# Kernel tuning notes

Measured on AMD Instinct MI355X. Metric: run time of the kernel, lower is better.

The kernel has to match this reference:

```python
import jax, jax.numpy as jnp
import numpy as np

NEG = -1e30       # log-space 'zero'
KD_FACTOR = 0.5   # self.kd_factor
KD_TEMP = 1.0     # self.kd_temp is never set in the original __init__; use 1.0
BLANK = 0         # torch CTCLoss default blank id


def ctc_loss(logits, targets, ilens, olens):
    """CTC negative log-likelihood, sum-reduced / B (matches builtin path:
    log_softmax + nn.CTCLoss(reduction='sum', zero_infinity=True) / batch).
    logits: [B,T,C]; targets: [B,L] label ids (no blanks); ilens, olens: [B]."""
    B, T, C = logits.shape
    L = targets.shape[1]
    S = 2 * L + 1
    lp = jax.nn.log_softmax(logits, axis=-1)                     # [B,T,C]
    # extended label sequence: blank, y1, blank, y2, ..., blank  -> [B,S]
    ext = jnp.zeros((B, S), dtype=targets.dtype).at[:, 1::2].set(targets)
    prev2 = jnp.pad(ext, ((0, 0), (2, 0)))[:, :S]
    allow2 = (ext != BLANK) & (ext != prev2) & (jnp.arange(S)[None, :] >= 2)
    # per-frame emission log-probs of extended labels: [T,B,S]
    emit = jnp.take_along_axis(lp, jnp.broadcast_to(ext[:, None, :], (B, T, S)), axis=2)
    emit = jnp.transpose(emit, (1, 0, 2))
    alpha0 = (jnp.full((B, S), NEG, dtype=lp.dtype)
              .at[:, 0].set(emit[0, :, 0])
              .at[:, 1].set(emit[0, :, 1]))

    def step(alpha, xs):
        e_t, t = xs
        s1 = jnp.pad(alpha, ((0, 0), (1, 0)), constant_values=NEG)[:, :S]
        s2 = jnp.where(allow2, jnp.pad(alpha, ((0, 0), (2, 0)), constant_values=NEG)[:, :S], NEG)
        m = jnp.maximum(jnp.maximum(alpha, s1), s2)
        new = m + jnp.log(jnp.exp(alpha - m) + jnp.exp(s1 - m) + jnp.exp(s2 - m)) + e_t
        # freeze alpha past each sample's input length -> alpha at t = ilen-1
        new = jnp.where((t < ilens)[:, None], new, alpha)
        return new, None

    alpha, _ = jax.lax.scan(step, alpha0, (emit[1:], jnp.arange(1, T)))
    end = 2 * olens                                              # last blank index
    bidx = jnp.arange(B)
    ll = jnp.logaddexp(alpha[bidx, end], alpha[bidx, end - 1])
    loss = -ll
    loss = jnp.where(loss > 1e20, 0.0, loss)                     # zero_infinity
    return loss.sum() / B


def kd_loss(logits, soft_logits, hlens):
    """Vectorized form of the per-sample ragged KD loop:
    sum_b -(softmax(soft[b,:h]/T) * log_softmax(logits[b,:h]/T)).sum() / B."""
    B, T, _ = logits.shape
    p = jax.nn.softmax(soft_logits / KD_TEMP, axis=-1)
    logq = jax.nn.log_softmax(logits / KD_TEMP, axis=-1)
    cxe = -(p * logq).sum(-1)                                    # [B,T]
    mask = jnp.arange(T)[None, :] < hlens[:, None]
    return jnp.where(mask, cxe, 0.0).sum() / B


def setup_inputs() -> dict:
    key = jax.random.key(0)
    k1, k2, k3, k4, k5, k6 = jax.random.split(key, 6)
    B, T, E, V, L = 16, 512, 512, 5000, 64
    hs_pad = jax.random.normal(k1, (B, T, E), jnp.float32)
    soft_logits = jax.random.normal(k2, (B, T, V), jnp.float32)
    W = jax.random.normal(k3, (E, V), jnp.float32) * 0.02
    b = jnp.zeros((V,), jnp.float32)
    hlens = jax.random.randint(k4, (B,), 300, T + 1)             # T >= 2L+1 guaranteed
    targets = jax.random.randint(k5, (B, L), 1, V)               # no blank labels
    olens = jax.random.randint(k6, (B,), 32, L + 1)
    return {"hs_pad": hs_pad, "soft_logits": soft_logits, "W": W, "b": b,
            "hlens": hlens, "targets": targets, "olens": olens}


def reference(hs_pad, soft_logits, W, b, hlens, targets, olens):
    # ctc_lo(F.dropout(hs_pad, p=0.0)) -> plain linear projection
    logits = hs_pad @ W + b                                      # [B,T,V]
    loss_ctc = ctc_loss(logits, targets, hlens, olens)
    loss_kd = kd_loss(logits, soft_logits, hlens)
    return KD_FACTOR * loss_kd + (1.0 - KD_FACTOR) * loss_ctc
```

## Files before the change

### kernel.cpp

```cpp
#include <hip/hip_runtime.h>
#include <math.h>

#define LOG2E 1.4426950408889634f
#define LN2 0.6931471805599453f

constexpr int B_ = 16;
constexpr int T_ = 512;
constexpr int E_ = 512;
constexpr int V_ = 5000;
constexpr int VP_ = 5120;
constexpr int L_ = 64;
constexpr int S_ = 2 * L_ + 1;
constexpr int SP_ = 132;

typedef __attribute__((ext_vector_type(8))) short bf16x8;
typedef __attribute__((ext_vector_type(4))) float f32x4;

#define GLOAD_LDS16(g, l)                                                              \
  __builtin_amdgcn_global_load_lds((const __attribute__((address_space(1))) void*)(g), \
                                   (__attribute__((address_space(3))) void*)(l), 16, 0, 0)

__device__ __forceinline__ unsigned short f2bf(float x) {
  unsigned int u = __float_as_uint(x);
  unsigned int r = (u + 0x7fffu + ((u >> 16) & 1u)) >> 16;
  return (unsigned short)r;
}
__device__ __forceinline__ float bf2f(unsigned int lo16) {
  return __uint_as_float(lo16 << 16);
}

__device__ __forceinline__ float hexp2(float x) { return __builtin_amdgcn_exp2f(x); }
__device__ __forceinline__ float hlog2(float x) { return __builtin_amdgcn_logf(x); }

__device__ __forceinline__ float dpp_shr1_zero(float v) {
  int s = __float_as_int(v);
  int bc = __builtin_amdgcn_update_dpp(0, s, 0x142, 0xF, 0xF, false);
  int r = __builtin_amdgcn_update_dpp(bc, s, 0x111, 0xF, 0xF, false);
  return __int_as_float(r);
}

template <int CTRL>
__device__ __forceinline__ float dpp_mv(float v) {
  int s = __float_as_int(v);
  return __int_as_float(__builtin_amdgcn_update_dpp(s, s, CTRL, 0xF, 0xF, false));
}

__device__ __forceinline__ float blockReduceF(float v, bool is_max, volatile float* red) {
  int tid = threadIdx.x, lane = tid & 63, wid = tid >> 6;
#pragma unroll
  for (int off = 32; off > 0; off >>= 1) {
    float o = __shfl_down(v, off, 64);
    v = is_max ? fmaxf(v, o) : (v + o);
  }
  __syncthreads();
  if (lane == 0) red[wid] = v;
  __syncthreads();
  float r = red[0];
#pragma unroll
  for (int w = 1; w < 4; ++w) r = is_max ? fmaxf(r, (float)red[w]) : (r + (float)red[w]);
  return r;
}

__global__ __launch_bounds__(256) void convA(const float* __restrict__ X,
                                             unsigned short* __restrict__ Y, int n4) {
  int i = blockIdx.x * 256 + threadIdx.x;
  if (i >= n4) return;
  float4 v = ((const float4*)X)[i];
  ushort4 o;
  o.x = f2bf(v.x); o.y = f2bf(v.y); o.z = f2bf(v.z); o.w = f2bf(v.w);
  ((ushort4*)Y)[i] = o;
}

__global__ __launch_bounds__(256) void convW(const float* __restrict__ W,
                                             unsigned short* __restrict__ Wt) {
  __shared__ float tile[32][33];
  int n0 = blockIdx.x * 32, k0 = blockIdx.y * 32;
  int tid = threadIdx.x;
  int tx = tid & 31, ty = tid >> 5;
#pragma unroll
  for (int p = 0; p < 4; ++p) {
    int k = k0 + ty + p * 8, n = n0 + tx;
    tile[ty + p * 8][tx] = (n < V_) ? W[(size_t)k * V_ + n] : 0.0f;
  }
  __syncthreads();
#pragma unroll
  for (int p = 0; p < 4; ++p) {
    int n = n0 + ty + p * 8, k = k0 + tx;
    Wt[(size_t)n * E_ + k] = f2bf(tile[tx][ty + p * 8]);
  }
}

__global__ __launch_bounds__(256) void gemm_mfma(const unsigned short* __restrict__ A,
                                                 const unsigned short* __restrict__ Wt,
                                                 const float* __restrict__ bias,
                                                 unsigned short* __restrict__ C) {
  __shared__ unsigned short As[128 * 32];
  __shared__ unsigned short Bs[128 * 32];
  int tid = threadIdx.x;
  int l = tid & 63, wid = tid >> 6;
  int lane15 = l & 15, lhalf = l >> 4;
  int wr = wid >> 1, wc = wid & 1;
  int bm = blockIdx.y * 128;
  int bn = blockIdx.x * 128;

  f32x4 acc[4][4] = {};

  int srow = l >> 2;
  int scol = (((l & 3) ^ ((l >> 3) & 3)) << 3);
  int rswz = ((lhalf ^ ((lane15 >> 1) & 3)) << 3);
  for (int k0 = 0; k0 < E_; k0 += 32) {
#pragma unroll
    for (int i = 0; i < 2; ++i) {
      int rb = wid * 32 + i * 16;
      GLOAD_LDS16(A + (size_t)(bm + rb + srow) * E_ + k0 + scol, &As[rb * 32]);
      GLOAD_LDS16(Wt + (size_t)(bn + rb + srow) * E_ + k0 + scol, &Bs[rb * 32]);
    }
    __syncthreads();
    bf16x8 af[4], bf[4];
#pragma unroll
    for (int m = 0; m < 4; ++m)
      af[m] = *(const bf16x8*)&As[(wr * 64 + m * 16 + lane15) * 32 + rswz];
#pragma unroll
    for (int n = 0; n < 4; ++n)
      bf[n] = *(const bf16x8*)&Bs[(wc * 64 + n * 16 + lane15) * 32 + rswz];
#pragma unroll
    for (int m = 0; m < 4; ++m)
#pragma unroll
      for (int n = 0; n < 4; ++n)
        acc[m][n] = __builtin_amdgcn_mfma_f32_16x16x32_bf16(af[m], bf[n], acc[m][n], 0, 0, 0);
    __syncthreads();
  }

#pragma unroll
  for (int n = 0; n < 4; ++n) {
    int col = bn + wc * 64 + n * 16 + lane15;
    float bv = (col < V_) ? bias[col] : 0.0f;
#pragma unroll
    for (int m = 0; m < 4; ++m) {
      int row0 = bm + wr * 64 + m * 16 + lhalf * 4;
#pragma unroll
      for (int j = 0; j < 4; ++j) {
        C[(size_t)(row0 + j) * VP_ + col] = f2bf(acc[m][n][j] + bv);
      }
    }
  }
}

__global__ __launch_bounds__(256) void row_fused(const unsigned short* __restrict__ Cc,
                                                 const float* __restrict__ soft,
                                                 const int* __restrict__ hlens,
                                                 const int* __restrict__ targets,
                                                 float* __restrict__ cxe,
                                                 float* __restrict__ emit, int r0) {
  int r = blockIdx.x;
  int row = r0 + r;
  int bidx = row >> 9;
  int t = row & (T_ - 1);
  const unsigned short* crow = Cc + (size_t)r * VP_;
  const uint4* lrow = (const uint4*)crow;
  const float4* srow = (const float4*)(soft + (size_t)row * V_);
  __shared__ float red[4];
  int tid = threadIdx.x;

  uint4 lu[3];
  float4 sv[3][2];
  bool valid[3];
#pragma unroll
  for (int k = 0; k < 3; ++k) {
    int slot = tid + k * 256;
    valid[k] = (slot < V_ / 8);
    if (valid[k]) {
      lu[k] = lrow[slot];
      sv[k][0] = srow[slot * 2];
      sv[k][1] = srow[slot * 2 + 1];
    }
  }

  float maxl = -INFINITY, maxs = -INFINITY;
#pragma unroll
  for (int k = 0; k < 3; ++k) {
    if (valid[k]) {
      unsigned int w0 = lu[k].x, w1 = lu[k].y, w2 = lu[k].z, w3 = lu[k].w;
      maxl = fmaxf(maxl, fmaxf(fmaxf(bf2f(w0 & 0xffffu), bf2f(w0 >> 16)),
                               fmaxf(bf2f(w1 & 0xffffu), bf2f(w1 >> 16))));
      maxl = fmaxf(maxl, fmaxf(fmaxf(bf2f(w2 & 0xffffu), bf2f(w2 >> 16)),
                               fmaxf(bf2f(w3 & 0xffffu), bf2f(w3 >> 16))));
      float4 a = sv[k][0], b = sv[k][1];
      maxs = fmaxf(maxs, fmaxf(fmaxf(a.x, a.y), fmaxf(a.z, a.w)));
      maxs = fmaxf(maxs, fmaxf(fmaxf(b.x, b.y), fmaxf(b.z, b.w)));
    }
  }
  maxl = blockReduceF(maxl, true, red);
  maxs = blockReduceF(maxs, true, red);

  float suml = 0.f, sums = 0.f, dot = 0.f;
#pragma unroll
  for (int k = 0; k < 3; ++k) {
    if (valid[k]) {
      float lv[8], ss[8];
      unsigned int w0 = lu[k].x, w1 = lu[k].y, w2 = lu[k].z, w3 = lu[k].w;
      lv[0] = bf2f(w0 & 0xffffu); lv[1] = bf2f(w0 >> 16);
      lv[2] = bf2f(w1 & 0xffffu); lv[3] = bf2f(w1 >> 16);
      lv[4] = bf2f(w2 & 0xffffu); lv[5] = bf2f(w2 >> 16);
      lv[6] = bf2f(w3 & 0xffffu); lv[7] = bf2f(w3 >> 16);
      float4 a = sv[k][0], b = sv[k][1];
      ss[0] = a.x; ss[1] = a.y; ss[2] = a.z; ss[3] = a.w;
      ss[4] = b.x; ss[5] = b.y; ss[6] = b.z; ss[7] = b.w;
#pragma unroll
      for (int j = 0; j < 8; ++j) {
        suml += hexp2((lv[j] - maxl) * LOG2E);
        float e = hexp2((ss[j] - maxs) * LOG2E);
        sums += e;
        dot = fmaf(e, lv[j], dot);
      }
    }
  }
  suml = blockReduceF(suml, false, red);
  sums = blockReduceF(sums, false, red);
  dot = blockReduceF(dot, false, red);

  float lse = maxl + hlog2(suml) * LN2;
  if (tid == 0) {
    cxe[row] = (t < hlens[bidx]) ? (lse - dot / sums) : 0.0f;
  }

  if (tid < 64) {
    int i0 = tid, i1 = tid + 64;
    int idx0 = (i0 & 1) ? targets[bidx * L_ + (i0 >> 1)] : 0;
    int idx1 = (i1 & 1) ? targets[bidx * L_ + (i1 >> 1)] : 0;
    float e0 = (bf2f(crow[idx0]) - lse) * LOG2E;
    float e1 = (bf2f(crow[idx1]) - lse) * LOG2E;
    float e2 = 0.f;
    if (tid == 0) e2 = (bf2f(crow[0]) - lse) * LOG2E;
    float m = fmaxf(e0, e1);
    if (tid == 0) m = fmaxf(m, e2);
#pragma unroll
    for (int off = 32; off > 0; off >>= 1) m = fmaxf(m, __shfl_xor(m, off, 64));
    float* erow = emit + ((size_t)bidx * T_ + t) * SP_;
    erow[i0] = hexp2(e0 - m);
    erow[i1] = hexp2(e1 - m);
    if (tid == 0) {
      erow[128] = hexp2(e2 - m);
      erow[130] = m;
    }
  }
}

__device__ __forceinline__ void pstep(float& a0, float& a1, float& a2, float allowf,
                                      float e0, float e1, float e2) {
  float ua1 = dpp_shr1_zero(a1);
  float n0 = (a0 + ua1) * e0;
  float n1 = fmaf(ua1, allowf, a0 + a1) * e1;
  float n2 = (a2 + a1) * e2;
  a0 = n0; a1 = n1; a2 = n2;
}

__device__ __forceinline__ void renorm(float& a0, float& a1, float& a2, float& shift,
                                       int lane) {
  float m = fmaxf(a0, a1);
  m = (lane == 63) ? fmaxf(m, a2) : m;
  m = fmaxf(m, dpp_mv<0xB1>(m));
  m = fmaxf(m, dpp_mv<0x4E>(m));
  m = fmaxf(m, dpp_mv<0x124>(m));
  m = fmaxf(m, dpp_mv<0x128>(m));
  m = fmaxf(m, __shfl_xor(m, 16, 64));
  m = fmaxf(m, __shfl_xor(m, 32, 64));
  m = fmaxf(m, 1e-35f);
  float rs = __builtin_amdgcn_rcpf(m) * 281474976710656.0f;
  a0 *= rs; a1 *= rs; a2 *= rs;
  shift -= hlog2(rs);
}

__global__ __launch_bounds__(64) void ctc_fwd(const float* __restrict__ emit,
                                              const int* __restrict__ hlens,
                                              const int* __restrict__ targets,
                                              const int* __restrict__ olens,
                                              float* __restrict__ ctc_out) {
  int b = blockIdx.x;
  int l = threadIdx.x;
  const float* Eb = emit + (size_t)b * T_ * SP_;
  float allowf = 0.f;
  if (l >= 1) allowf = (targets[b * L_ + l] != targets[b * L_ + l - 1]) ? 1.0f : 0.0f;

  float a0, a1, a2, shift;
  {
    float2 e01 = *(const float2*)(Eb + 2 * l);
    float4 x = *(const float4*)(Eb + 128);
    a0 = (l == 0) ? e01.x : 0.0f;
    a1 = (l == 0) ? e01.y : 0.0f;
    a2 = 0.0f;
    shift = x.z;
  }
  int ilen = hlens[b];

#define LDE(tt) (*(const float2*)(Eb + (size_t)(tt) * SP_ + 2 * l))
#define LDX(tt) (*(const float4*)(Eb + (size_t)(tt) * SP_ + 128))

  float2 c0 = LDE(1), c1 = LDE(2), c2 = LDE(3), c3 = LDE(4);
  float2 c4 = LDE(5), c5 = LDE(6), c6 = LDE(7), c7 = LDE(8);
  float4 x0 = LDX(1), x1 = LDX(2), x2 = LDX(3), x3 = LDX(4);
  float4 x4 = LDX(5), x5 = LDX(6), x6 = LDX(7), x7 = LDX(8);

  int t = 1;
  for (; t + 7 <= ilen - 1; t += 8) {
    float2 p0 = LDE(t + 8), p1 = LDE(t + 9), p2 = LDE(t + 10), p3 = LDE(t + 11);
    float2 p4 = LDE(t + 12), p5 = LDE(t + 13), p6 = LDE(t + 14), p7 = LDE(t + 15);
    float4 q0 = LDX(t + 8), q1 = LDX(t + 9), q2 = LDX(t + 10), q3 = LDX(t + 11);
    float4 q4 = LDX(t + 12), q5 = LDX(t + 13), q6 = LDX(t + 14), q7 = LDX(t + 15);
    pstep(a0, a1, a2, allowf, c0.x, c0.y, x0.x);
    pstep(a0, a1, a2, allowf, c1.x, c1.y, x1.x);
    pstep(a0, a1, a2, allowf, c2.x, c2.y, x2.x);
    pstep(a0, a1, a2, allowf, c3.x, c3.y, x3.x);
    pstep(a0, a1, a2, allowf, c4.x, c4.y, x4.x);
    pstep(a0, a1, a2, allowf, c5.x, c5.y, x5.x);
    pstep(a0, a1, a2, allowf, c6.x, c6.y, x6.x);
    pstep(a0, a1, a2, allowf, c7.x, c7.y, x7.x);
    shift += ((x0.z + x1.z) + (x2.z + x3.z)) + ((x4.z + x5.z) + (x6.z + x7.z));
    renorm(a0, a1, a2, shift, l);
    c0 = p0; c1 = p1; c2 = p2; c3 = p3; c4 = p4; c5 = p5; c6 = p6; c7 = p7;
    x0 = q0; x1 = q1; x2 = q2; x3 = q3; x4 = q4; x5 = q5; x6 = q6; x7 = q7;
  }
  int rem = ilen - t;
  if (rem > 0) { pstep(a0, a1, a2, allowf, c0.x, c0.y, x0.x); shift += x0.z; }
  if (rem > 1) { pstep(a0, a1, a2, allowf, c1.x, c1.y, x1.x); shift += x1.z; }
  if (rem > 2) { pstep(a0, a1, a2, allowf, c2.x, c2.y, x2.x); shift += x2.z; }
  if (rem > 3) { pstep(a0, a1, a2, allowf, c3.x, c3.y, x3.x); shift += x3.z; }
  if (rem > 4) { pstep(a0, a1, a2, allowf, c4.x, c4.y, x4.x); shift += x4.z; }
  if (rem > 5) { pstep(a0, a1, a2, allowf, c5.x, c5.y, x5.x); shift += x5.z; }
  if (rem > 6) { pstep(a0, a1, a2, allowf, c6.x, c6.y, x6.x); shift += x6.z; }
#undef LDE
#undef LDX

  int end = 2 * olens[b];
  float aE = (end == 128) ? __shfl(a2, 63, 64) : __shfl(a0, end >> 1, 64);
  float aE1 = __shfl(a1, (end >> 1) - 1, 64);
  if (l == 0) {
    float p = aE + aE1;
    float ll = (hlog2(p) + shift) * LN2;
    float loss = -ll;
    if (!(loss <= 1e20f)) loss = 0.0f;
    ctc_out[b] = loss;
  }
}

__global__ __launch_bounds__(256) void final_reduce(const float* __restrict__ cxe,
                                                    const float* __restrict__ ctco,
                                                    float* __restrict__ out) {
  __shared__ float red[4];
  float s = 0.f;
  for (int i = threadIdx.x; i < B_ * T_; i += 256) s += cxe[i];
  s = blockReduceF(s, false, red);
  if (threadIdx.x == 0) {
    float c = 0.f;
    for (int b = 0; b < B_; ++b) c += ctco[b];
    out[0] = 0.5f * (s / (float)B_) + 0.5f * (c / (float)B_);
  }
}

extern "C" void kernel_launch(void* const* d_in, const int* in_sizes, int n_in,
                              void* d_out, int out_size, void* d_ws, size_t ws_size,
                              hipStream_t stream) {
  const float* hs = (const float*)d_in[0];
  const float* soft = (const float*)d_in[1];
  const float* W = (const float*)d_in[2];
  const float* bias = (const float*)d_in[3];
  const int* hlens = (const int*)d_in[4];
  const int* targets = (const int*)d_in[5];
  const int* olens = (const int*)d_in[6];
  float* out = (float*)d_out;

  int total = B_ * T_;
  size_t emit_n = (size_t)(total + 16) * SP_;
  float* emit = (float*)d_ws;
  float* cxe = emit + emit_n;
  float* ctco = cxe + (size_t)total;
  unsigned short* Abf = (unsigned short*)(ctco + 16);
  unsigned short* Wt = Abf + (size_t)total * E_;
  unsigned short* logits = Wt + (size_t)VP_ * E_;
  size_t used = (size_t)((char*)logits - (char*)d_ws);
  size_t avail = (ws_size > used) ? (ws_size - used) : 0;
  int max_rows = (int)(avail / ((size_t)VP_ * sizeof(unsigned short)));
  int chunk = max_rows & ~127;
  if (chunk > total) chunk = total;
  if (chunk < 128) chunk = 128;

  dim3 blk(256);
  {
    int n4 = total * E_ / 4;
    hipLaunchKernelGGL(convA, dim3((n4 + 255) / 256), blk, 0, stream, hs, Abf, n4);
    hipLaunchKernelGGL(convW, dim3(VP_ / 32, E_ / 32), blk, 0, stream, W, Wt);
  }

  for (int r0 = 0; r0 < total; r0 += chunk) {
    int mc = total - r0;
    if (mc > chunk) mc = chunk;
    dim3 g1(VP_ / 128, mc / 128);
    hipLaunchKernelGGL(gemm_mfma, g1, blk, 0, stream, Abf + (size_t)r0 * E_, Wt, bias, logits);
    hipLaunchKernelGGL(row_fused, dim3(mc), blk, 0, stream, logits, soft, hlens, targets,
                       cxe, emit, r0);
  }
  hipLaunchKernelGGL(ctc_fwd, dim3(B_), dim3(64), 0, stream, emit, hlens, targets, olens, ctco);
  hipLaunchKernelGGL(final_reduce, dim3(1), blk, 0, stream, cxe, ctco, out);
}
```

Before: 178.5 us.

## Skip padded frames past hlens, double-buffer GEMM LDS, merge conversion kernels

The GEMM now returns early for 128-row tiles that lie entirely past each sample's input length and skips storing rows beyond it. The row kernel also exits early for frames with t >= hlens, writing zero to the KD term. The GEMM k-loop double-buffers its LDS tiles so the next tile's global-to-LDS load is issued while the current one is computed, and the two fp32-to-bf16 conversion kernels are merged into one launch. The risk is that CTC emit rows for skipped frames are left unwritten; this is only safe if the CTC forward never reads alpha past ilen-1.

```diff
diff --git a/kernel.cpp b/kernel.cpp
--- a/kernel.cpp
+++ b/kernel.cpp
@@ -61,20 +61,25 @@
   return r;
 }
 
-__global__ __launch_bounds__(256) void convA(const float* __restrict__ X,
-                                             unsigned short* __restrict__ Y, int n4) {
-  int i = blockIdx.x * 256 + threadIdx.x;
-  if (i >= n4) return;
-  float4 v = ((const float4*)X)[i];
-  ushort4 o;
-  o.x = f2bf(v.x); o.y = f2bf(v.y); o.z = f2bf(v.z); o.w = f2bf(v.w);
-  ((ushort4*)Y)[i] = o;
-}
-
-__global__ __launch_bounds__(256) void convW(const float* __restrict__ W,
-                                             unsigned short* __restrict__ Wt) {
+__global__ __launch_bounds__(256) void conv_all(const float* __restrict__ X,
+                                                unsigned short* __restrict__ Y, int n4,
+                                                int nAblk,
+                                                const float* __restrict__ W,
+                                                unsigned short* __restrict__ Wt) {
+  int bid = blockIdx.x;
+  if (bid < nAblk) {
+    int i = bid * 256 + threadIdx.x;
+    if (i >= n4) return;
+    float4 v = ((const float4*)X)[i];
+    ushort4 o;
+    o.x = f2bf(v.x); o.y = f2bf(v.y); o.z = f2bf(v.z); o.w = f2bf(v.w);
+    ((ushort4*)Y)[i] = o;
+    return;
+  }
   __shared__ float tile[32][33];
-  int n0 = blockIdx.x * 32, k0 = blockIdx.y * 32;
+  int wblk = bid - nAblk;
+  int n0 = (wblk % (VP_ / 32)) * 32;
+  int k0 = (wblk / (VP_ / 32)) * 32;
   int tid = threadIdx.x;
   int tx = tid & 31, ty = tid >> 5;
 #pragma unroll
@@ -93,43 +98,61 @@
 __global__ __launch_bounds__(256) void gemm_mfma(const unsigned short* __restrict__ A,
                                                  const unsigned short* __restrict__ Wt,
                                                  const float* __restrict__ bias,
-                                                 unsigned short* __restrict__ C) {
-  __shared__ unsigned short As[128 * 32];
-  __shared__ unsigned short Bs[128 * 32];
+                                                 const int* __restrict__ hlens,
+                                                 unsigned short* __restrict__ C, int r0) {
+  __shared__ unsigned short As[2][128 * 32];
+  __shared__ unsigned short Bs[2][128 * 32];
   int tid = threadIdx.x;
   int l = tid & 63, wid = tid >> 6;
   int lane15 = l & 15, lhalf = l >> 4;
   int wr = wid >> 1, wc = wid & 1;
   int bm = blockIdx.y * 128;
   int bn = blockIdx.x * 128;
+  int bmAbs = r0 + bm;
+  int hl = hlens[bmAbs >> 9];
+  int tIn = bmAbs & (T_ - 1);
+  if (tIn >= hl) return;
 
   f32x4 acc[4][4] = {};
 
   int srow = l >> 2;
   int scol = (((l & 3) ^ ((l >> 3) & 3)) << 3);
   int rswz = ((lhalf ^ ((lane15 >> 1) & 3)) << 3);
+
+  const unsigned short* Arow = A + (size_t)bm * E_ + scol;
+  const unsigned short* Brow = Wt + (size_t)bn * E_ + scol;
+
+#define STAGE(buf, k0)                                                              \
+  {                                                                                 \
+    _Pragma("unroll") for (int i = 0; i < 2; ++i) {                                 \
+      int rb = wid * 32 + i * 16;                                                   \
+      GLOAD_LDS16(Arow + (size_t)(rb + srow) * E_ + (k0), &As[buf][rb * 32]);       \
+      GLOAD_LDS16(Brow + (size_t)(rb + srow) * E_ + (k0), &Bs[buf][rb * 32]);       \
+    }                                                                               \
+  }
+
+  STAGE(0, 0);
+  __syncthreads();
+  int cur = 0;
+#pragma unroll
   for (int k0 = 0; k0 < E_; k0 += 32) {
-#pragma unroll
-    for (int i = 0; i < 2; ++i) {
-      int rb = wid * 32 + i * 16;
-      GLOAD_LDS16(A + (size_t)(bm + rb + srow) * E_ + k0 + scol, &As[rb * 32]);
-      GLOAD_LDS16(Wt + (size_t)(bn + rb + srow) * E_ + k0 + scol, &Bs[rb * 32]);
-    }
-    __syncthreads();
+    if (k0 + 32 < E_) STAGE(cur ^ 1, k0 + 32);
     bf16x8 af[4], bf[4];
 #pragma unroll
     for (int m = 0; m < 4; ++m)
-      af[m] = *(const bf16x8*)&As[(wr * 64 + m * 16 + lane15) * 32 + rswz];
+      af[m] = *(const bf16x8*)&As[cur][(wr * 64 + m * 16 + lane15) * 32 + rswz];
 #pragma unroll
     for (int n = 0; n < 4; ++n)
-      bf[n] = *(const bf16x8*)&Bs[(wc * 64 + n * 16 + lane15) * 32 + rswz];
+      bf[n] = *(const bf16x8*)&Bs[cur][(wc * 64 + n * 16 + lane15) * 32 + rswz];
 #pragma unroll
     for (int m = 0; m < 4; ++m)
 #pragma unroll
       for (int n = 0; n < 4; ++n)
         acc[m][n] = __builtin_amdgcn_mfma_f32_16x16x32_bf16(af[m], bf[n], acc[m][n], 0, 0, 0);
     __syncthreads();
-  }
+    cur ^= 1;
+  }
+#undef STAGE
 
 #pragma unroll
   for (int n = 0; n < 4; ++n) {
@@ -137,10 +160,11 @@
     float bv = (col < V_) ? bias[col] : 0.0f;
 #pragma unroll
     for (int m = 0; m < 4; ++m) {
-      int row0 = bm + wr * 64 + m * 16 + lhalf * 4;
+      int rloc = wr * 64 + m * 16 + lhalf * 4;
 #pragma unroll
       for (int j = 0; j < 4; ++j) {
-        C[(size_t)(row0 + j) * VP_ + col] = f2bf(acc[m][n][j] + bv);
+        if (tIn + rloc + j < hl)
+          C[(size_t)(bm + rloc + j) * VP_ + col] = f2bf(acc[m][n][j] + bv);
       }
     }
   }
@@ -156,11 +180,16 @@
   int row = r0 + r;
   int bidx = row >> 9;
   int t = row & (T_ - 1);
+  int tid = threadIdx.x;
+  int hl = hlens[bidx];
+  if (t >= hl) {
+    if (tid == 0) cxe[row] = 0.0f;
+    return;
+  }
   const unsigned short* crow = Cc + (size_t)r * VP_;
   const uint4* lrow = (const uint4*)crow;
   const float4* srow = (const float4*)(soft + (size_t)row * V_);
   __shared__ float red[4];
-  int tid = threadIdx.x;
 
   uint4 lu[3];
   float4 sv[3][2];
@@ -221,7 +250,7 @@
 
   float lse = maxl + hlog2(suml) * LN2;
   if (tid == 0) {
-    cxe[row] = (t < hlens[bidx]) ? (lse - dot / sums) : 0.0f;
+    cxe[row] = lse - dot / sums;
   }
 
   if (tid < 64) {
@@ -387,15 +416,18 @@
   dim3 blk(256);
   {
     int n4 = total * E_ / 4;
-    hipLaunchKernelGGL(convA, dim3((n4 + 255) / 256), blk, 0, stream, hs, Abf, n4);
-    hipLaunchKernelGGL(convW, dim3(VP_ / 32, E_ / 32), blk, 0, stream, W, Wt);
+    int nAblk = (n4 + 255) / 256;
+    int nWblk = (VP_ / 32) * (E_ / 32);
+    hipLaunchKernelGGL(conv_all, dim3(nAblk + nWblk), blk, 0, stream, hs, Abf, n4,
+                       nAblk, W, Wt);
   }
 
   for (int r0 = 0; r0 < total; r0 += chunk) {
     int mc = total - r0;
     if (mc > chunk) mc = chunk;
     dim3 g1(VP_ / 128, mc / 128);
-    hipLaunchKernelGGL(gemm_mfma, g1, blk, 0, stream, Abf + (size_t)r0 * E_, Wt, bias, logits);
+    hipLaunchKernelGGL(gemm_mfma, g1, blk, 0, stream, Abf + (size_t)r0 * E_, Wt, bias,
+                       hlens, logits, r0);
     hipLaunchKernelGGL(row_fused, dim3(mc), blk, 0, stream, logits, soft, hlens, targets,
                        cxe, emit, r0);
   }
```

New measurement: 180.0 us. Within noise of the previous version (+0.8%).
